# Kernel optimization log

Hardware: AMD Instinct MI355X
Metric: run time of the kernel (lower is better)

The kernel has to match this reference:

```python
import jax, jax.numpy as jnp
import numpy as np

T, B, C, K, E = 1024, 32, 1024, 1024, 16  # seq, batch, d_model(=in=out), key_dim, n_experts
LOSS_SCALE = 0.01


def setup_inputs() -> dict:
    key0 = jax.random.key(0)
    k0, k1, k2, k3 = jax.random.split(key0, 4)
    x = jax.random.normal(k0, (T, B, C), dtype=jnp.float32)
    key = jax.random.normal(k1, (1, B, K), dtype=jnp.float32)
    bnd = float(np.sqrt(6.0 / (K + E)))  # xavier_uniform for assign Linear
    assign_w = jax.random.uniform(k2, (K, E), jnp.float32, -bnd, bnd)
    assign_b = jnp.zeros((E,), jnp.float32)
    a = float(np.sqrt(6.0) / (C + C))  # dynamic_init_method=1
    pw_w1 = jax.random.uniform(k3, (E, C * C), jnp.float32, -a, a)
    return {"x": x, "key": key, "assign_w": assign_w, "assign_b": assign_b, "pw_w1": pw_w1}


def reference(x, key, assign_w, assign_b, pw_w1):
    Tn, Bn, Cn = x.shape
    Tr = key.shape[0]  # key is provided -> Tr = 1 (one routing decision per batch element)
    En = assign_b.shape[0]
    # routing: softmax over experts (gumbel_tau=0 -> plain softmax branch)
    logits = key.reshape(Tr * Bn, -1) @ assign_w + assign_b  # (Tr*B, E)
    resp = jax.nn.softmax(logits, axis=-1)
    importance = resp.sum(axis=0)  # (E,)
    loss = LOSS_SCALE * jnp.std(importance, ddof=1) / jnp.mean(importance)  # torch.std is unbiased
    # mix expert weights: (Tr*B, E) @ (E, O*I) -> per-token/sentence weight matrix
    w = (resp @ pw_w1).reshape(Tr, Bn, Cn, Cn)  # (Tr, B, O, I)
    # batched matvec, broadcasting Tr=1 over T (sum over size-1 axis r == broadcast)
    y = jnp.einsum('rboi,tbi->tbo', w, x)
    return x + y, loss
```

## Files before the change

### kernel.cpp

```cpp
#include <hip/hip_runtime.h>
#include <stdint.h>


#define TBC   (1024*32*1024)

typedef __attribute__((ext_vector_type(8))) __bf16 bf16x8;
typedef __attribute__((ext_vector_type(4))) float  floatx4;

__device__ __forceinline__ unsigned short f2bf(float f) {
  unsigned u = __float_as_uint(f);
  unsigned r = u + 0x7fffu + ((u >> 16) & 1u);
  return (unsigned short)(r >> 16);
}
__device__ __forceinline__ float bf2f(unsigned short u) {
  return __uint_as_float(((unsigned)u) << 16);
}

__device__ __forceinline__ void async16(const void* g, void* l) {
  __builtin_amdgcn_global_load_lds(
      (const __attribute__((address_space(1))) void*)(unsigned long long)(uintptr_t)g,
      (__attribute__((address_space(3))) void*)(unsigned int)(uintptr_t)l,
      16, 0, 0);
}

__global__ __launch_bounds__(256) void routing_kernel(
    const float* __restrict__ key, const float* __restrict__ aw,
    const float* __restrict__ ab, float* __restrict__ resp) {
  __shared__ float part[16][17];
  __shared__ float logit[16];
  const int b = blockIdx.x;
  const int tid = threadIdx.x;
  const int e = tid & 15, ks = tid >> 4;
  const float* kb = key + b * 1024 + ks * 64;
  float acc = 0.f;
  #pragma unroll 8
  for (int k = 0; k < 64; ++k)
    acc = fmaf(kb[k], aw[(ks * 64 + k) * 16 + e], acc);
  part[e][ks] = acc;
  __syncthreads();
  if (tid < 16) {
    float s = ab[tid];
    #pragma unroll
    for (int j = 0; j < 16; ++j) s += part[tid][j];
    logit[tid] = s;
  }
  __syncthreads();
  if (tid < 16) {
    float m = logit[0];
    #pragma unroll
    for (int j = 1; j < 16; ++j) m = fmaxf(m, logit[j]);
    float s = 0.f;
    #pragma unroll
    for (int j = 0; j < 16; ++j) s += expf(logit[j] - m);
    resp[b * 16 + tid] = expf(logit[tid] - m) / s;
  }
}

__global__ void loss_kernel(const float* __restrict__ resp, float* __restrict__ loss_out) {
  __shared__ float imp[16];
  const int tid = threadIdx.x;
  if (tid < 16) {
    float s = 0.f;
    for (int bb = 0; bb < 32; ++bb) s += resp[bb * 16 + tid];
    imp[tid] = s;
  }
  __syncthreads();
  if (tid == 0) {
    float mu = 0.f;
    for (int j = 0; j < 16; ++j) mu += imp[j];
    mu *= (1.f / 16.f);
    float var = 0.f;
    for (int j = 0; j < 16; ++j) { float d = imp[j] - mu; var += d * d; }
    var *= (1.f / 15.f);
    loss_out[0] = 0.01f * sqrtf(var) / mu;
  }
}

__global__ __launch_bounds__(256) void prep_kernel(
    const float4* __restrict__ x, ushort4* __restrict__ xb,
    const float4* __restrict__ pw, const float* __restrict__ resp,
    ushort4* __restrict__ W) {
  const int tid = threadIdx.x;
  if (blockIdx.x < 32768) {
    const int i = blockIdx.x * 256 + tid;
    float4 v = x[i];
    ushort4 o;
    o.x = f2bf(v.x); o.y = f2bf(v.y); o.z = f2bf(v.z); o.w = f2bf(v.w);
    xb[i] = o;
  } else {
    __shared__ float rs[512];
    rs[tid] = resp[tid];
    rs[tid + 256] = resp[tid + 256];
    __syncthreads();
    const int p = (blockIdx.x - 32768) * 256 + tid;
    float4 v[16];
    #pragma unroll
    for (int e = 0; e < 16; ++e) v[e] = pw[e * 262144 + p];
    #pragma unroll
    for (int b = 0; b < 32; ++b) {
      float ax = 0.f, ay = 0.f, az = 0.f, aww = 0.f;
      #pragma unroll
      for (int e = 0; e < 16; ++e) {
        const float r = rs[b * 16 + e];
        ax = fmaf(r, v[e].x, ax); ay = fmaf(r, v[e].y, ay);
        az = fmaf(r, v[e].z, az); aww = fmaf(r, v[e].w, aww);
      }
      ushort4 o;
      o.x = f2bf(ax); o.y = f2bf(ay); o.z = f2bf(az); o.w = f2bf(aww);
      W[(size_t)b * 262144 + p] = o;
    }
  }
}

__global__ __launch_bounds__(256, 2) void gemm_kernel(
    const unsigned short* __restrict__ xb,
    const unsigned short* __restrict__ Wb,
    float* __restrict__ out) {
  __shared__ unsigned short lds[3 * 128 * 64];
  const int tid  = threadIdx.x;
  const int lane = tid & 63;
  const int wave = tid >> 6;
  const int wm = wave & 1, wn = wave >> 1;

  const int gid   = blockIdx.x;
  const int xcd   = gid & 7;
  const int local = gid >> 3;
  const int b     = xcd * 4 + (local >> 5);
  const int sub   = local & 31;
  const int o0    = (sub & 7) * 128;
  const int t0    = (sub >> 3) * 256;

  unsigned short* ldsA0 = lds;
  unsigned short* ldsA1 = lds + 128 * 64;
  unsigned short* ldsB  = lds + 2 * 128 * 64;

  const unsigned short* gA0[4];
  const unsigned short* gA1[4];
  const unsigned short* gB[4];
  #pragma unroll
  for (int j = 0; j < 4; ++j) {
    const int s  = j * 256 + tid;
    const int r  = s >> 3;
    const int cg = (s & 7) ^ (r & 7);
    gA0[j] = xb + (size_t)(t0 + r)       * 32768 + (size_t)b * 1024 + cg * 8;
    gA1[j] = xb + (size_t)(t0 + 128 + r) * 32768 + (size_t)b * 1024 + cg * 8;
    gB[j]  = Wb + (size_t)b * 1048576 + (size_t)(o0 + r) * 1024 + cg * 8;
  }

  floatx4 acc[2][4][4];
  #pragma unroll
  for (int th = 0; th < 2; ++th)
    #pragma unroll
    for (int mi = 0; mi < 4; ++mi)
      #pragma unroll
      for (int ni = 0; ni < 4; ++ni)
        acc[th][mi][ni] = floatx4{0.f, 0.f, 0.f, 0.f};

  for (int kt = 0; kt < 1024; kt += 64) {
    if (kt) __syncthreads();
    #pragma unroll
    for (int j = 0; j < 4; ++j) {
      const int dst = (j * 256 + wave * 64) * 8;
      async16(gA0[j], ldsA0 + dst);
      async16(gA1[j], ldsA1 + dst);
      async16(gB[j],  ldsB  + dst);
      gA0[j] += 64; gA1[j] += 64; gB[j] += 64;
    }
    __syncthreads();
    #pragma unroll
    for (int kk = 0; kk < 2; ++kk) {
      bf16x8 bfr[4];
      #pragma unroll
      for (int ni = 0; ni < 4; ++ni) {
        const int r = wn * 64 + ni * 16 + (lane & 15);
        const int slot = (kk * 4 + (lane >> 4)) ^ (r & 7);
        bfr[ni] = *(const bf16x8*)(ldsB + r * 64 + slot * 8);
      }
      #pragma unroll
      for (int th = 0; th < 2; ++th) {
        unsigned short* ldsA = th ? ldsA1 : ldsA0;
        bf16x8 af[4];
        #pragma unroll
        for (int mi = 0; mi < 4; ++mi) {
          const int r = wm * 64 + mi * 16 + (lane & 15);
          const int slot = (kk * 4 + (lane >> 4)) ^ (r & 7);
          af[mi] = *(const bf16x8*)(ldsA + r * 64 + slot * 8);
        }
        #pragma unroll
        for (int mi = 0; mi < 4; ++mi)
          #pragma unroll
          for (int ni = 0; ni < 4; ++ni)
            acc[th][mi][ni] = __builtin_amdgcn_mfma_f32_16x16x32_bf16(af[mi], bfr[ni], acc[th][mi][ni], 0, 0, 0);
      }
    }
  }

  #pragma unroll
  for (int th = 0; th < 2; ++th) {
    #pragma unroll
    for (int mi = 0; mi < 4; ++mi) {
      const int tb = t0 + th * 128 + wm * 64 + mi * 16 + (lane >> 4) * 4;
      #pragma unroll
      for (int ni = 0; ni < 4; ++ni) {
        const int o = o0 + wn * 64 + ni * 16 + (lane & 15);
        #pragma unroll
        for (int v = 0; v < 4; ++v) {
          const size_t idx = (size_t)(tb + v) * 32768 + (size_t)b * 1024 + o;
          out[idx] = acc[th][mi][ni][v] + bf2f(xb[idx]);
        }
      }
    }
  }
}

extern "C" void kernel_launch(void* const* d_in, const int* in_sizes, int n_in,
                              void* d_out, int out_size, void* d_ws, size_t ws_size,
                              hipStream_t stream) {
  const float* x   = (const float*)d_in[0];
  const float* key = (const float*)d_in[1];
  const float* aw  = (const float*)d_in[2];
  const float* ab  = (const float*)d_in[3];
  const float* pw  = (const float*)d_in[4];
  float* out = (float*)d_out;

  char* ws = (char*)d_ws;
  unsigned short* Wb = (unsigned short*)ws;
  unsigned short* xb = (unsigned short*)(ws + 67108864);
  float* resp        = (float*)(ws + 134217728);

  routing_kernel<<<32, 256, 0, stream>>>(key, aw, ab, resp);
  loss_kernel<<<1, 64, 0, stream>>>(resp, out + TBC);
  prep_kernel<<<33792, 256, 0, stream>>>((const float4*)x, (ushort4*)xb,
                                         (const float4*)pw, resp, (ushort4*)Wb);
  gemm_kernel<<<1024, 256, 0, stream>>>(xb, Wb, out);
}
```

Baseline: 396.4 us.

## Restructure GEMM into 4-stage async LDS pipeline with 256x256 tiles

The GEMM now uses 512-thread blocks, each computing a 256x256 tile. K steps are 32 wide and staged through a 4-deep ring of LDS buffers loaded with async global-to-LDS copies and explicit vmcnt waits. This replaces the single-buffer load-sync-compute loop, so memory latency can overlap with MFMA work. It also raises MFMA priority with setprio and uses a new swizzle. The x-to-bf16 conversion in prep is coarsened so each thread does 16 float4s, cutting the block count. The changes trade higher register and LDS pressure, and hand-tuned waitcnt counts that must match the issued loads exactly, for better overlap and reuse.

Result: slower. 410.0 us (+3.4%).

```diff
diff --git a/kernel.cpp b/kernel.cpp
--- a/kernel.cpp
+++ b/kernel.cpp
@@ -6,6 +6,8 @@
 
 typedef __attribute__((ext_vector_type(8))) __bf16 bf16x8;
 typedef __attribute__((ext_vector_type(4))) float  floatx4;
+
+#define XSWZ(r) ((((r) & 3) ^ (((r) >> 2) & 3)))
 
 __device__ __forceinline__ unsigned short f2bf(float f) {
   unsigned u = __float_as_uint(f);
@@ -81,18 +83,22 @@
     const float4* __restrict__ pw, const float* __restrict__ resp,
     ushort4* __restrict__ W) {
   const int tid = threadIdx.x;
-  if (blockIdx.x < 32768) {
-    const int i = blockIdx.x * 256 + tid;
-    float4 v = x[i];
-    ushort4 o;
-    o.x = f2bf(v.x); o.y = f2bf(v.y); o.z = f2bf(v.z); o.w = f2bf(v.w);
-    xb[i] = o;
+  if (blockIdx.x < 2048) {
+    const int base = blockIdx.x * 256 + tid;
+    #pragma unroll
+    for (int j = 0; j < 16; ++j) {
+      const int i = base + j * 524288;
+      float4 v = x[i];
+      ushort4 o;
+      o.x = f2bf(v.x); o.y = f2bf(v.y); o.z = f2bf(v.z); o.w = f2bf(v.w);
+      xb[i] = o;
+    }
   } else {
     __shared__ float rs[512];
     rs[tid] = resp[tid];
     rs[tid + 256] = resp[tid + 256];
     __syncthreads();
-    const int p = (blockIdx.x - 32768) * 256 + tid;
+    const int p = (blockIdx.x - 2048) * 256 + tid;
     float4 v[16];
     #pragma unroll
     for (int e = 0; e < 16; ++e) v[e] = pw[e * 262144 + p];
@@ -112,102 +118,114 @@
   }
 }
 
-__global__ __launch_bounds__(256, 2) void gemm_kernel(
+__global__ __launch_bounds__(512, 2) void gemm_kernel(
     const unsigned short* __restrict__ xb,
     const unsigned short* __restrict__ Wb,
     float* __restrict__ out) {
-  __shared__ unsigned short lds[3 * 128 * 64];
+  __shared__ unsigned short lds[4][2][8192];
   const int tid  = threadIdx.x;
   const int lane = tid & 63;
   const int wave = tid >> 6;
-  const int wm = wave & 1, wn = wave >> 1;
+  const int wm = wave >> 2;
+  const int wn = wave & 3;
 
   const int gid   = blockIdx.x;
   const int xcd   = gid & 7;
   const int local = gid >> 3;
-  const int b     = xcd * 4 + (local >> 5);
-  const int sub   = local & 31;
-  const int o0    = (sub & 7) * 128;
-  const int t0    = (sub >> 3) * 256;
-
-  unsigned short* ldsA0 = lds;
-  unsigned short* ldsA1 = lds + 128 * 64;
-  unsigned short* ldsB  = lds + 2 * 128 * 64;
-
-  const unsigned short* gA0[4];
-  const unsigned short* gA1[4];
-  const unsigned short* gB[4];
+  const int b     = xcd * 4 + (local >> 4);
+  const int sub   = local & 15;
+  const int t0    = (sub >> 2) * 256;
+  const int o0    = (sub & 3) * 256;
+
+  const unsigned short* gA[2];
+  const unsigned short* gB[2];
   #pragma unroll
-  for (int j = 0; j < 4; ++j) {
-    const int s  = j * 256 + tid;
-    const int r  = s >> 3;
-    const int cg = (s & 7) ^ (r & 7);
-    gA0[j] = xb + (size_t)(t0 + r)       * 32768 + (size_t)b * 1024 + cg * 8;
-    gA1[j] = xb + (size_t)(t0 + 128 + r) * 32768 + (size_t)b * 1024 + cg * 8;
-    gB[j]  = Wb + (size_t)b * 1048576 + (size_t)(o0 + r) * 1024 + cg * 8;
-  }
-
-  floatx4 acc[2][4][4];
+  for (int j = 0; j < 2; ++j) {
+    const int s  = j * 512 + tid;
+    const int r  = s >> 2;
+    const int cg = (s & 3) ^ XSWZ(r);
+    gA[j] = xb + (size_t)(t0 + r) * 32768 + (size_t)b * 1024 + cg * 8;
+    gB[j] = Wb + (size_t)b * 1048576 + (size_t)(o0 + r) * 1024 + cg * 8;
+  }
+
+  floatx4 acc[8][4];
   #pragma unroll
-  for (int th = 0; th < 2; ++th)
-    #pragma unroll
-    for (int mi = 0; mi < 4; ++mi)
-      #pragma unroll
-      for (int ni = 0; ni < 4; ++ni)
-        acc[th][mi][ni] = floatx4{0.f, 0.f, 0.f, 0.f};
-
-  for (int kt = 0; kt < 1024; kt += 64) {
-    if (kt) __syncthreads();
-    #pragma unroll
-    for (int j = 0; j < 4; ++j) {
-      const int dst = (j * 256 + wave * 64) * 8;
-      async16(gA0[j], ldsA0 + dst);
-      async16(gA1[j], ldsA1 + dst);
-      async16(gB[j],  ldsB  + dst);
-      gA0[j] += 64; gA1[j] += 64; gB[j] += 64;
-    }
-    __syncthreads();
-    #pragma unroll
-    for (int kk = 0; kk < 2; ++kk) {
-      bf16x8 bfr[4];
-      #pragma unroll
-      for (int ni = 0; ni < 4; ++ni) {
-        const int r = wn * 64 + ni * 16 + (lane & 15);
-        const int slot = (kk * 4 + (lane >> 4)) ^ (r & 7);
-        bfr[ni] = *(const bf16x8*)(ldsB + r * 64 + slot * 8);
+  for (int a = 0; a < 8; ++a)
+    #pragma unroll
+    for (int ni = 0; ni < 4; ++ni)
+      acc[a][ni] = floatx4{0.f, 0.f, 0.f, 0.f};
+
+  auto stage = [&](int bufi) {
+    #pragma unroll
+    for (int j = 0; j < 2; ++j) {
+      const int dst = (j * 512 + wave * 64) * 8;
+      async16(gA[j], &lds[bufi][0][dst]);
+      async16(gB[j], &lds[bufi][1][dst]);
+      gA[j] += 32; gB[j] += 32;
+    }
+  };
+
+  auto compute = [&](int bufi) {
+    const unsigned short* lA = &lds[bufi][0][0];
+    const unsigned short* lB = &lds[bufi][1][0];
+    bf16x8 bfr[4];
+    #pragma unroll
+    for (int ni = 0; ni < 4; ++ni) {
+      const int r = wn * 64 + ni * 16 + (lane & 15);
+      const int slot = (lane >> 4) ^ XSWZ(r);
+      bfr[ni] = *(const bf16x8*)(lB + r * 32 + slot * 8);
+    }
+    #pragma unroll
+    for (int half = 0; half < 2; ++half) {
+      bf16x8 afr[4];
+      #pragma unroll
+      for (int mi = 0; mi < 4; ++mi) {
+        const int r = wm * 128 + half * 64 + mi * 16 + (lane & 15);
+        const int slot = (lane >> 4) ^ XSWZ(r);
+        afr[mi] = *(const bf16x8*)(lA + r * 32 + slot * 8);
       }
-      #pragma unroll
-      for (int th = 0; th < 2; ++th) {
-        unsigned short* ldsA = th ? ldsA1 : ldsA0;
-        bf16x8 af[4];
+      __builtin_amdgcn_s_setprio(1);
+      #pragma unroll
+      for (int mi = 0; mi < 4; ++mi)
         #pragma unroll
-        for (int mi = 0; mi < 4; ++mi) {
-          const int r = wm * 64 + mi * 16 + (lane & 15);
-          const int slot = (kk * 4 + (lane >> 4)) ^ (r & 7);
-          af[mi] = *(const bf16x8*)(ldsA + r * 64 + slot * 8);
-        }
-        #pragma unroll
-        for (int mi = 0; mi < 4; ++mi)
-          #pragma unroll
-          for (int ni = 0; ni < 4; ++ni)
-            acc[th][mi][ni] = __builtin_amdgcn_mfma_f32_16x16x32_bf16(af[mi], bfr[ni], acc[th][mi][ni], 0, 0, 0);
-      }
-    }
+        for (int ni = 0; ni < 4; ++ni)
+          acc[half * 4 + mi][ni] = __builtin_amdgcn_mfma_f32_16x16x32_bf16(
+              afr[mi], bfr[ni], acc[half * 4 + mi][ni], 0, 0, 0);
+      __builtin_amdgcn_s_setprio(0);
+      if (half == 0) __builtin_amdgcn_s_barrier();
+    }
+  };
+
+  stage(0); stage(1); stage(2);
+
+  for (int t = 0; t < 32; ++t) {
+    if (t <= 28) {
+      stage((t + 3) & 3);
+      asm volatile("s_waitcnt vmcnt(12)" ::: "memory");
+    } else if (t == 29) {
+      asm volatile("s_waitcnt vmcnt(8)" ::: "memory");
+    } else if (t == 30) {
+      asm volatile("s_waitcnt vmcnt(4)" ::: "memory");
+    } else {
+      asm volatile("s_waitcnt vmcnt(0)" ::: "memory");
+    }
+    __builtin_amdgcn_s_barrier();
+    asm volatile("" ::: "memory");
+    compute(t & 3);
+    asm volatile("s_waitcnt lgkmcnt(0)" ::: "memory");
+    __builtin_amdgcn_s_barrier();
   }
 
   #pragma unroll
-  for (int th = 0; th < 2; ++th) {
-    #pragma unroll
-    for (int mi = 0; mi < 4; ++mi) {
-      const int tb = t0 + th * 128 + wm * 64 + mi * 16 + (lane >> 4) * 4;
-      #pragma unroll
-      for (int ni = 0; ni < 4; ++ni) {
-        const int o = o0 + wn * 64 + ni * 16 + (lane & 15);
-        #pragma unroll
-        for (int v = 0; v < 4; ++v) {
-          const size_t idx = (size_t)(tb + v) * 32768 + (size_t)b * 1024 + o;
-          out[idx] = acc[th][mi][ni][v] + bf2f(xb[idx]);
-        }
+  for (int a = 0; a < 8; ++a) {
+    const int tb = t0 + wm * 128 + (a >> 2) * 64 + (a & 3) * 16 + (lane >> 4) * 4;
+    #pragma unroll
+    for (int ni = 0; ni < 4; ++ni) {
+      const int o = o0 + wn * 64 + ni * 16 + (lane & 15);
+      #pragma unroll
+      for (int v = 0; v < 4; ++v) {
+        const size_t idx = (size_t)(tb + v) * 32768 + (size_t)b * 1024 + o;
+        out[idx] = acc[a][ni][v] + bf2f(xb[idx]);
       }
     }
   }
@@ -230,7 +248,7 @@
 
   routing_kernel<<<32, 256, 0, stream>>>(key, aw, ab, resp);
   loss_kernel<<<1, 64, 0, stream>>>(resp, out + TBC);
-  prep_kernel<<<33792, 256, 0, stream>>>((const float4*)x, (ushort4*)xb,
-                                         (const float4*)pw, resp, (ushort4*)Wb);
-  gemm_kernel<<<1024, 256, 0, stream>>>(xb, Wb, out);
-}
+  prep_kernel<<<3072, 256, 0, stream>>>((const float4*)x, (ushort4*)xb,
+                                        (const float4*)pw, resp, (ushort4*)Wb);
+  gemm_kernel<<<512, 512, 0, stream>>>(xb, Wb, out);
+}
```
